# Kernel tuning notes

Hardware: AMD Instinct MI355X
Metric: run time of the kernel (lower is better)

The kernel has to match this reference:

```python
import jax, jax.numpy as jnp
import numpy as np

N_NODES = 50000
D_FEAT = 128
N_EDGES = 600000
HIDDEN = 256


def setup_inputs() -> dict:
    key = jax.random.key(0)
    k1, k2, k3, k4 = jax.random.split(key, 4)
    nodes = jax.random.normal(k1, (N_NODES, D_FEAT), dtype=jnp.float32)
    senders = jax.random.randint(k2, (N_EDGES,), 0, N_NODES, dtype=jnp.int32)
    receivers = jax.random.randint(k3, (N_EDGES,), 0, N_NODES, dtype=jnp.int32)
    # Dense(hidden): input dim = 2*D_FEAT (concat of aggregated + self features)
    W = jax.random.normal(k4, (2 * D_FEAT, HIDDEN), dtype=jnp.float32) / np.sqrt(2 * D_FEAT)
    b = jnp.zeros((HIDDEN,), dtype=jnp.float32)
    return {"nodes": nodes, "senders": senders, "receivers": receivers, "W": W, "b": b}


def reference(nodes, senders, receivers, W, b):
    n = nodes.shape[0]
    # segment_mean: gather sender features, scatter-sum onto receivers, divide by counts
    gathered = nodes[senders]                                    # [E, D]
    sums = jax.ops.segment_sum(gathered, receivers, num_segments=n)  # [N, D]
    counts = jax.ops.segment_sum(
        jnp.ones((senders.shape[0],), dtype=nodes.dtype), receivers, num_segments=n
    )                                                            # [N]
    h_e = sums / jnp.maximum(counts, 1.0)[:, None]               # mean (0 for empty segments)
    h = jnp.concatenate([h_e, nodes], axis=-1)                   # [N, 2D]
    out = jax.nn.relu(h @ W + b)                                 # [N, HIDDEN]
    return out
```

## Files before the change

### kernel.cpp

```cpp
#include <hip/hip_runtime.h>
#include <hip/hip_bf16.h>

#define N_NODES 50000
#define D_FEAT  128
#define N_EDGES 600000
#define HIDDEN  256
#define K_DIM   256

#define BUCKET   64
#define M_TILE   32
#define NTILES   1563
#define H_STRIDE 264

typedef __attribute__((ext_vector_type(8))) short bf16x8;
typedef __attribute__((ext_vector_type(4))) float f32x4;

__device__ __forceinline__ unsigned short f32_to_bf16(float f) {
    unsigned int u = __float_as_uint(f);
    unsigned int r = (u + 0x7fffu + ((u >> 16) & 1u)) >> 16;
    return (unsigned short)r;
}
__device__ __forceinline__ unsigned int pack_bf16x2(float lo, float hi) {
    return (unsigned int)f32_to_bf16(lo) | ((unsigned int)f32_to_bf16(hi) << 16);
}

__global__ __launch_bounds__(256) void build_and_repack(
    const int* __restrict__ senders,
    const int* __restrict__ receivers,
    const float* __restrict__ W,
    unsigned int* __restrict__ cnt,
    unsigned short* __restrict__ edges16,
    unsigned short* __restrict__ Wp) {
    const int gid = blockIdx.x * 256 + threadIdx.x;
    const int gsz = gridDim.x * 256;
    for (int e = gid; e < N_EDGES; e += gsz) {
        int r = receivers[e];
        unsigned int slot = atomicAdd(&cnt[r], 1u);
        if (slot < (unsigned int)BUCKET)
            edges16[(size_t)r * BUCKET + slot] = (unsigned short)senders[e];
    }
    for (int t = gid; t < 65536; t += gsz) {
        int kt = t >> 13;
        int n  = (t >> 5) & 255;
        int q  = (t >> 3) & 3;
        int j  = t & 7;
        int k  = kt * 32 + q * 8 + j;
        Wp[t] = f32_to_bf16(W[k * 256 + n]);
    }
}

__global__ __launch_bounds__(256) void gather_mean_gemm(
    const float* __restrict__ nodes,
    const unsigned int* __restrict__ cnt,
    const unsigned short* __restrict__ edges16,
    const unsigned short* __restrict__ Wp,
    const float* __restrict__ bias,
    float* __restrict__ out) {
    __shared__ __align__(16) unsigned int h32[M_TILE * (H_STRIDE / 2)];

    const int m0   = blockIdx.x * M_TILE;
    const int tid  = threadIdx.x;
    const int wave = tid >> 6;
    const int lane = tid & 63;

    for (int i = 0; i < 8; i++) {
        int row = wave * 8 + i;
        int m   = m0 + row;
        float s0 = 0.f, s1 = 0.f, p0 = 0.f, p1 = 0.f;
        float q0 = 0.f, q1 = 0.f, r0 = 0.f, r1 = 0.f;
        float self0 = 0.f, self1 = 0.f;
        unsigned int ec = 0;
        if (m < N_NODES) {
            unsigned int c = cnt[m];
            ec = c < (unsigned int)BUCKET ? c : (unsigned int)BUCKET;
            const unsigned int* ep =
                (const unsigned int*)(edges16 + (size_t)m * BUCKET);
            unsigned int np = ec >> 1;
            unsigned int pj = 0;
            for (; pj + 4 <= np; pj += 4) {
                unsigned int w0 = ep[pj + 0], w1 = ep[pj + 1];
                unsigned int w2 = ep[pj + 2], w3 = ep[pj + 3];
                const float2 va = *(const float2*)(nodes + (size_t)(w0 & 0xffffu) * D_FEAT + lane * 2);
                const float2 vb = *(const float2*)(nodes + (size_t)(w0 >> 16)     * D_FEAT + lane * 2);
                const float2 vc = *(const float2*)(nodes + (size_t)(w1 & 0xffffu) * D_FEAT + lane * 2);
                const float2 vd = *(const float2*)(nodes + (size_t)(w1 >> 16)     * D_FEAT + lane * 2);
                const float2 ve = *(const float2*)(nodes + (size_t)(w2 & 0xffffu) * D_FEAT + lane * 2);
                const float2 vf = *(const float2*)(nodes + (size_t)(w2 >> 16)     * D_FEAT + lane * 2);
                const float2 vg = *(const float2*)(nodes + (size_t)(w3 & 0xffffu) * D_FEAT + lane * 2);
                const float2 vh = *(const float2*)(nodes + (size_t)(w3 >> 16)     * D_FEAT + lane * 2);
                s0 += va.x; s1 += va.y;  p0 += vb.x; p1 += vb.y;
                q0 += vc.x; q1 += vc.y;  r0 += vd.x; r1 += vd.y;
                s0 += ve.x; s1 += ve.y;  p0 += vf.x; p1 += vf.y;
                q0 += vg.x; q1 += vg.y;  r0 += vh.x; r1 += vh.y;
            }
            for (; pj < np; pj++) {
                unsigned int w0 = ep[pj];
                const float2 va = *(const float2*)(nodes + (size_t)(w0 & 0xffffu) * D_FEAT + lane * 2);
                const float2 vb = *(const float2*)(nodes + (size_t)(w0 >> 16)     * D_FEAT + lane * 2);
                s0 += va.x; s1 += va.y;  p0 += vb.x; p1 += vb.y;
            }
            if (ec & 1u) {
                unsigned int sid = edges16[(size_t)m * BUCKET + (ec - 1)];
                const float2 va = *(const float2*)(nodes + (size_t)sid * D_FEAT + lane * 2);
                s0 += va.x; s1 += va.y;
            }
            const float2 sv = *(const float2*)(nodes + (size_t)m * D_FEAT + lane * 2);
            self0 = sv.x; self1 = sv.y;
        }
        float inv = 1.0f / fmaxf((float)ec, 1.0f);
        float a0 = (s0 + p0 + q0 + r0) * inv;
        float a1 = (s1 + p1 + q1 + r1) * inv;
        h32[row * (H_STRIDE / 2) + lane]      = pack_bf16x2(a0, a1);
        h32[row * (H_STRIDE / 2) + 64 + lane] = pack_bf16x2(self0, self1);
    }
    __syncthreads();

    const unsigned short* h = (const unsigned short*)h32;
    const int nbase = wave * 64;
    const int rsel  = lane & 15;
    const int quad  = lane >> 4;

    f32x4 acc[2][4] = {};

    for (int kk = 0; kk < K_DIM; kk += 32) {
        bf16x8 a[2], bw[4];
        #pragma unroll
        for (int mt = 0; mt < 2; mt++) {
            const unsigned short* pa =
                &h[(mt * 16 + rsel) * H_STRIDE + kk + quad * 8];
            a[mt] = *(const bf16x8*)pa;
        }
        int kt = kk >> 5;
        #pragma unroll
        for (int nt = 0; nt < 4; nt++) {
            int n = nbase + nt * 16 + rsel;
            bw[nt] = *(const bf16x8*)&Wp[kt * 8192 + n * 32 + quad * 8];
        }
        #pragma unroll
        for (int mt = 0; mt < 2; mt++)
            #pragma unroll
            for (int nt = 0; nt < 4; nt++)
                acc[mt][nt] = __builtin_amdgcn_mfma_f32_16x16x32_bf16(
                    a[mt], bw[nt], acc[mt][nt], 0, 0, 0);
    }

    #pragma unroll
    for (int nt = 0; nt < 4; nt++) {
        int n = nbase + nt * 16 + rsel;
        float bn = bias[n];
        #pragma unroll
        for (int mt = 0; mt < 2; mt++) {
            #pragma unroll
            for (int r = 0; r < 4; r++) {
                int m = m0 + mt * 16 + quad * 4 + r;
                if (m < N_NODES) {
                    float v = acc[mt][nt][r] + bn;
                    out[(size_t)m * HIDDEN + n] = fmaxf(v, 0.0f);
                }
            }
        }
    }
}

extern "C" void kernel_launch(void* const* d_in, const int* in_sizes, int n_in,
                              void* d_out, int out_size, void* d_ws, size_t ws_size,
                              hipStream_t stream) {
    const float* nodes     = (const float*)d_in[0];
    const int*   senders   = (const int*)d_in[1];
    const int*   receivers = (const int*)d_in[2];
    const float* W         = (const float*)d_in[3];
    const float* bias      = (const float*)d_in[4];
    float*       out       = (float*)d_out;

    unsigned int*   cnt     = (unsigned int*)d_ws;
    unsigned short* edges16 = (unsigned short*)(cnt + N_NODES);
    unsigned short* Wp      = edges16 + (size_t)N_NODES * BUCKET;

    hipMemsetAsync(cnt, 0, (size_t)N_NODES * sizeof(unsigned int), stream);

    build_and_repack<<<dim3((N_EDGES + 255) / 256), dim3(256), 0, stream>>>(
        senders, receivers, W, cnt, edges16, Wp);

    gather_mean_gemm<<<dim3(NTILES), dim3(256), 0, stream>>>(
        nodes, cnt, edges16, Wp, bias, out);
}
```

Before: 199.6 us.

## Gather from bf16 node copy with tile-flattened edge list and LDS atomics

```diff
diff --git a/kernel.cpp b/kernel.cpp
--- a/kernel.cpp
+++ b/kernel.cpp
@@ -10,7 +10,6 @@
 #define BUCKET   64
 #define M_TILE   32
 #define NTILES   1563
-#define H_STRIDE 264
 
 typedef __attribute__((ext_vector_type(8))) short bf16x8;
 typedef __attribute__((ext_vector_type(4))) float f32x4;
@@ -20,16 +19,21 @@
     unsigned int r = (u + 0x7fffu + ((u >> 16) & 1u)) >> 16;
     return (unsigned short)r;
 }
+__device__ __forceinline__ float bf16_to_f32(unsigned short u) {
+    return __uint_as_float(((unsigned int)u) << 16);
+}
 __device__ __forceinline__ unsigned int pack_bf16x2(float lo, float hi) {
     return (unsigned int)f32_to_bf16(lo) | ((unsigned int)f32_to_bf16(hi) << 16);
 }
 
-__global__ __launch_bounds__(256) void build_and_repack(
+__global__ __launch_bounds__(256) void build_conv_repack(
     const int* __restrict__ senders,
     const int* __restrict__ receivers,
+    const float* __restrict__ nodes,
     const float* __restrict__ W,
     unsigned int* __restrict__ cnt,
     unsigned short* __restrict__ edges16,
+    unsigned int* __restrict__ nb,
     unsigned short* __restrict__ Wp) {
     const int gid = blockIdx.x * 256 + threadIdx.x;
     const int gsz = gridDim.x * 256;
@@ -39,6 +43,10 @@
         if (slot < (unsigned int)BUCKET)
             edges16[(size_t)r * BUCKET + slot] = (unsigned short)senders[e];
     }
+    for (int p = gid; p < N_NODES * 64; p += gsz) {
+        const float2 v = *(const float2*)(nodes + (size_t)p * 2);
+        nb[p] = pack_bf16x2(v.x, v.y);
+    }
     for (int t = gid; t < 65536; t += gsz) {
         int kt = t >> 13;
         int n  = (t >> 5) & 255;
@@ -49,88 +57,119 @@
     }
 }
 
-__global__ __launch_bounds__(256) void gather_mean_gemm(
-    const float* __restrict__ nodes,
+__global__ __launch_bounds__(256, 4) void gather_mean_gemm(
+    const unsigned int* __restrict__ nb,
     const unsigned int* __restrict__ cnt,
     const unsigned short* __restrict__ edges16,
     const unsigned short* __restrict__ Wp,
     const float* __restrict__ bias,
     float* __restrict__ out) {
-    __shared__ __align__(16) unsigned int h32[M_TILE * (H_STRIDE / 2)];
+    __shared__ __align__(16) float hacc[M_TILE * 132];
+    __shared__ __align__(16) unsigned int shared2[M_TILE * 68];
+    __shared__ unsigned int cn[M_TILE];
+    __shared__ unsigned int pref[M_TILE + 1];
+    __shared__ float invdeg[M_TILE];
 
     const int m0   = blockIdx.x * M_TILE;
     const int tid  = threadIdx.x;
     const int wave = tid >> 6;
     const int lane = tid & 63;
 
-    for (int i = 0; i < 8; i++) {
-        int row = wave * 8 + i;
-        int m   = m0 + row;
-        float s0 = 0.f, s1 = 0.f, p0 = 0.f, p1 = 0.f;
-        float q0 = 0.f, q1 = 0.f, r0 = 0.f, r1 = 0.f;
-        float self0 = 0.f, self1 = 0.f;
-        unsigned int ec = 0;
+    for (int i = tid; i < M_TILE * 132; i += 256) hacc[i] = 0.f;
+    if (tid < M_TILE) {
+        int m = m0 + tid;
+        unsigned int c = 0;
         if (m < N_NODES) {
-            unsigned int c = cnt[m];
-            ec = c < (unsigned int)BUCKET ? c : (unsigned int)BUCKET;
-            const unsigned int* ep =
-                (const unsigned int*)(edges16 + (size_t)m * BUCKET);
-            unsigned int np = ec >> 1;
-            unsigned int pj = 0;
-            for (; pj + 4 <= np; pj += 4) {
-                unsigned int w0 = ep[pj + 0], w1 = ep[pj + 1];
-                unsigned int w2 = ep[pj + 2], w3 = ep[pj + 3];
-                const float2 va = *(const float2*)(nodes + (size_t)(w0 & 0xffffu) * D_FEAT + lane * 2);
-                const float2 vb = *(const float2*)(nodes + (size_t)(w0 >> 16)     * D_FEAT + lane * 2);
-                const float2 vc = *(const float2*)(nodes + (size_t)(w1 & 0xffffu) * D_FEAT + lane * 2);
-                const float2 vd = *(const float2*)(nodes + (size_t)(w1 >> 16)     * D_FEAT + lane * 2);
-                const float2 ve = *(const float2*)(nodes + (size_t)(w2 & 0xffffu) * D_FEAT + lane * 2);
-                const float2 vf = *(const float2*)(nodes + (size_t)(w2 >> 16)     * D_FEAT + lane * 2);
-                const float2 vg = *(const float2*)(nodes + (size_t)(w3 & 0xffffu) * D_FEAT + lane * 2);
-                const float2 vh = *(const float2*)(nodes + (size_t)(w3 >> 16)     * D_FEAT + lane * 2);
-                s0 += va.x; s1 += va.y;  p0 += vb.x; p1 += vb.y;
-                q0 += vc.x; q1 += vc.y;  r0 += vd.x; r1 += vd.y;
-                s0 += ve.x; s1 += ve.y;  p0 += vf.x; p1 += vf.y;
-                q0 += vg.x; q1 += vg.y;  r0 += vh.x; r1 += vh.y;
-            }
-            for (; pj < np; pj++) {
-                unsigned int w0 = ep[pj];
-                const float2 va = *(const float2*)(nodes + (size_t)(w0 & 0xffffu) * D_FEAT + lane * 2);
-                const float2 vb = *(const float2*)(nodes + (size_t)(w0 >> 16)     * D_FEAT + lane * 2);
-                s0 += va.x; s1 += va.y;  p0 += vb.x; p1 += vb.y;
-            }
-            if (ec & 1u) {
-                unsigned int sid = edges16[(size_t)m * BUCKET + (ec - 1)];
-                const float2 va = *(const float2*)(nodes + (size_t)sid * D_FEAT + lane * 2);
-                s0 += va.x; s1 += va.y;
-            }
-            const float2 sv = *(const float2*)(nodes + (size_t)m * D_FEAT + lane * 2);
-            self0 = sv.x; self1 = sv.y;
-        }
-        float inv = 1.0f / fmaxf((float)ec, 1.0f);
-        float a0 = (s0 + p0 + q0 + r0) * inv;
-        float a1 = (s1 + p1 + q1 + r1) * inv;
-        h32[row * (H_STRIDE / 2) + lane]      = pack_bf16x2(a0, a1);
-        h32[row * (H_STRIDE / 2) + 64 + lane] = pack_bf16x2(self0, self1);
-    }
-    __syncthreads();
-
-    const unsigned short* h = (const unsigned short*)h32;
+            c = cnt[m];
+            if (c > (unsigned int)BUCKET) c = (unsigned int)BUCKET;
+        }
+        cn[tid] = c;
+        invdeg[tid] = 1.0f / fmaxf((float)c, 1.0f);
+    }
+    __syncthreads();
+    if (tid == 0) {
+        unsigned int run = 0;
+        for (int r = 0; r < M_TILE; r++) { pref[r] = run; run += cn[r]; }
+        pref[M_TILE] = run;
+    }
+    __syncthreads();
+
+    unsigned int* eflat = shared2;
+    {
+        int r  = tid >> 3, st = tid & 7;
+        unsigned int c = cn[r], base = pref[r];
+        size_t eb = (size_t)(m0 + r) * BUCKET;
+        for (unsigned int s = st; s < c; s += 8)
+            eflat[base + s] = ((unsigned int)r << 16) | edges16[eb + s];
+    }
+    __syncthreads();
+
+    const unsigned short* nb16 = (const unsigned short*)nb;
+    const int total = pref[M_TILE];
+    for (int base = wave * 16; base < total; base += 64) {
+        int nEdge = total - base; if (nEdge > 16) nEdge = 16;
+        unsigned int desc[16];
+        unsigned short flo[16], fhi[16];
+        #pragma unroll
+        for (int j = 0; j < 16; j++) {
+            if (j < nEdge) {
+                desc[j] = eflat[base + j];
+                size_t sa = (size_t)(desc[j] & 0xffffu) * 128;
+                flo[j] = nb16[sa + lane];
+                fhi[j] = nb16[sa + 64 + lane];
+            }
+        }
+        #pragma unroll
+        for (int j = 0; j < 16; j++) {
+            if (j < nEdge) {
+                int r = (int)(desc[j] >> 16);
+                atomicAdd(&hacc[r * 132 + lane],      bf16_to_f32(flo[j]));
+                atomicAdd(&hacc[r * 132 + 64 + lane], bf16_to_f32(fhi[j]));
+            }
+        }
+    }
+    __syncthreads();
+
+    for (int i = tid; i < M_TILE * 128; i += 256) {
+        int r = i >> 7, c = i & 127;
+        hacc[r * 132 + c] *= invdeg[r];
+    }
+    for (int i = tid; i < M_TILE * 64; i += 256) {
+        int r = i >> 6, c = i & 63;
+        int m = m0 + r;
+        shared2[r * 68 + c] = (m < N_NODES) ? nb[(size_t)m * 64 + c] : 0u;
+    }
+    __syncthreads();
+
+    const unsigned short* hs16 = (const unsigned short*)shared2;
     const int nbase = wave * 64;
     const int rsel  = lane & 15;
     const int quad  = lane >> 4;
 
     f32x4 acc[2][4] = {};
 
-    for (int kk = 0; kk < K_DIM; kk += 32) {
+    #pragma unroll
+    for (int kt = 0; kt < 8; kt++) {
         bf16x8 a[2], bw[4];
         #pragma unroll
         for (int mt = 0; mt < 2; mt++) {
-            const unsigned short* pa =
-                &h[(mt * 16 + rsel) * H_STRIDE + kk + quad * 8];
-            a[mt] = *(const bf16x8*)pa;
-        }
-        int kt = kk >> 5;
+            int row = mt * 16 + rsel;
+            if (kt < 4) {
+                const float* pa = &hacc[row * 132 + kt * 32 + quad * 8];
+                f32x4 vlo = *(const f32x4*)pa;
+                f32x4 vhi = *(const f32x4*)(pa + 4);
+                union { bf16x8 v; unsigned short u[8]; } tmp;
+                #pragma unroll
+                for (int j = 0; j < 4; j++) {
+                    tmp.u[j]     = f32_to_bf16(vlo[j]);
+                    tmp.u[4 + j] = f32_to_bf16(vhi[j]);
+                }
+                a[mt] = tmp.v;
+            } else {
+                a[mt] = *(const bf16x8*)
+                    &hs16[row * 136 + (kt - 4) * 32 + quad * 8];
+            }
+        }
         #pragma unroll
         for (int nt = 0; nt < 4; nt++) {
             int n = nbase + nt * 16 + rsel;
@@ -174,13 +213,14 @@
 
     unsigned int*   cnt     = (unsigned int*)d_ws;
     unsigned short* edges16 = (unsigned short*)(cnt + N_NODES);
-    unsigned short* Wp      = edges16 + (size_t)N_NODES * BUCKET;
+    unsigned int*   nb      = (unsigned int*)(edges16 + (size_t)N_NODES * BUCKET);
+    unsigned short* Wp      = (unsigned short*)(nb + (size_t)N_NODES * 64);
 
     hipMemsetAsync(cnt, 0, (size_t)N_NODES * sizeof(unsigned int), stream);
 
-    build_and_repack<<<dim3((N_EDGES + 255) / 256), dim3(256), 0, stream>>>(
-        senders, receivers, W, cnt, edges16, Wp);
+    build_conv_repack<<<dim3(4096), dim3(256), 0, stream>>>(
+        senders, receivers, nodes, W, cnt, edges16, nb, Wp);
 
     gather_mean_gemm<<<dim3(NTILES), dim3(256), 0, stream>>>(
-        nodes, cnt, edges16, Wp, bias, out);
-}
+        nb, cnt, edges16, Wp, bias, out);
+}
```

Result: slower. 592.5 us (+196.8%).

## Convert node features to bf16 once and gather in padded 16-wide batches

Applied to the files above, without the earlier changes.

```diff
diff --git a/kernel.cpp b/kernel.cpp
--- a/kernel.cpp
+++ b/kernel.cpp
@@ -8,6 +8,7 @@
 #define K_DIM   256
 
 #define BUCKET   64
+#define ZERO_ROW 50000
 #define M_TILE   32
 #define NTILES   1563
 #define H_STRIDE 264
@@ -23,13 +24,21 @@
 __device__ __forceinline__ unsigned int pack_bf16x2(float lo, float hi) {
     return (unsigned int)f32_to_bf16(lo) | ((unsigned int)f32_to_bf16(hi) << 16);
 }
-
-__global__ __launch_bounds__(256) void build_and_repack(
+__device__ __forceinline__ float bf_lo(unsigned int v) {
+    return __uint_as_float(v << 16);
+}
+__device__ __forceinline__ float bf_hi(unsigned int v) {
+    return __uint_as_float(v & 0xffff0000u);
+}
+
+__global__ __launch_bounds__(256) void build_conv_repack(
     const int* __restrict__ senders,
     const int* __restrict__ receivers,
+    const float* __restrict__ nodes,
     const float* __restrict__ W,
+    unsigned short* __restrict__ edges16,
     unsigned int* __restrict__ cnt,
-    unsigned short* __restrict__ edges16,
+    unsigned int* __restrict__ nb,
     unsigned short* __restrict__ Wp) {
     const int gid = blockIdx.x * 256 + threadIdx.x;
     const int gsz = gridDim.x * 256;
@@ -39,6 +48,11 @@
         if (slot < (unsigned int)BUCKET)
             edges16[(size_t)r * BUCKET + slot] = (unsigned short)senders[e];
     }
+    for (int p = gid; p < N_NODES * 64; p += gsz) {
+        const float2 v = *(const float2*)(nodes + (size_t)p * 2);
+        nb[p] = pack_bf16x2(v.x, v.y);
+    }
+    if (gid < 64) nb[(size_t)ZERO_ROW * 64 + gid] = 0u;
     for (int t = gid; t < 65536; t += gsz) {
         int kt = t >> 13;
         int n  = (t >> 5) & 255;
@@ -50,7 +64,7 @@
 }
 
 __global__ __launch_bounds__(256) void gather_mean_gemm(
-    const float* __restrict__ nodes,
+    const unsigned int* __restrict__ nb,
     const unsigned int* __restrict__ cnt,
     const unsigned short* __restrict__ edges16,
     const unsigned short* __restrict__ Wp,
@@ -68,50 +82,67 @@
         int m   = m0 + row;
         float s0 = 0.f, s1 = 0.f, p0 = 0.f, p1 = 0.f;
         float q0 = 0.f, q1 = 0.f, r0 = 0.f, r1 = 0.f;
-        float self0 = 0.f, self1 = 0.f;
-        unsigned int ec = 0;
+        unsigned int selfp = 0u;
+        unsigned int c = 0;
         if (m < N_NODES) {
-            unsigned int c = cnt[m];
-            ec = c < (unsigned int)BUCKET ? c : (unsigned int)BUCKET;
+            c = cnt[m];
+            if (c > (unsigned int)BUCKET) c = (unsigned int)BUCKET;
             const unsigned int* ep =
                 (const unsigned int*)(edges16 + (size_t)m * BUCKET);
-            unsigned int np = ec >> 1;
-            unsigned int pj = 0;
-            for (; pj + 4 <= np; pj += 4) {
-                unsigned int w0 = ep[pj + 0], w1 = ep[pj + 1];
-                unsigned int w2 = ep[pj + 2], w3 = ep[pj + 3];
-                const float2 va = *(const float2*)(nodes + (size_t)(w0 & 0xffffu) * D_FEAT + lane * 2);
-                const float2 vb = *(const float2*)(nodes + (size_t)(w0 >> 16)     * D_FEAT + lane * 2);
-                const float2 vc = *(const float2*)(nodes + (size_t)(w1 & 0xffffu) * D_FEAT + lane * 2);
-                const float2 vd = *(const float2*)(nodes + (size_t)(w1 >> 16)     * D_FEAT + lane * 2);
-                const float2 ve = *(const float2*)(nodes + (size_t)(w2 & 0xffffu) * D_FEAT + lane * 2);
-                const float2 vf = *(const float2*)(nodes + (size_t)(w2 >> 16)     * D_FEAT + lane * 2);
-                const float2 vg = *(const float2*)(nodes + (size_t)(w3 & 0xffffu) * D_FEAT + lane * 2);
-                const float2 vh = *(const float2*)(nodes + (size_t)(w3 >> 16)     * D_FEAT + lane * 2);
-                s0 += va.x; s1 += va.y;  p0 += vb.x; p1 += vb.y;
-                q0 += vc.x; q1 += vc.y;  r0 += vd.x; r1 += vd.y;
-                s0 += ve.x; s1 += ve.y;  p0 += vf.x; p1 += vf.y;
-                q0 += vg.x; q1 += vg.y;  r0 += vh.x; r1 += vh.y;
+            unsigned int cp = (c + 15u) & ~15u;
+            for (unsigned int s = 0; s < cp; s += 16) {
+                unsigned int w0 = ep[(s >> 1) + 0], w1 = ep[(s >> 1) + 1];
+                unsigned int w2 = ep[(s >> 1) + 2], w3 = ep[(s >> 1) + 3];
+                unsigned int w4 = ep[(s >> 1) + 4], w5 = ep[(s >> 1) + 5];
+                unsigned int w6 = ep[(s >> 1) + 6], w7 = ep[(s >> 1) + 7];
+                unsigned int id0  = (s + 0  < c) ? (w0 & 0xffffu) : ZERO_ROW;
+                unsigned int id1  = (s + 1  < c) ? (w0 >> 16)     : ZERO_ROW;
+                unsigned int id2  = (s + 2  < c) ? (w1 & 0xffffu) : ZERO_ROW;
+                unsigned int id3  = (s + 3  < c) ? (w1 >> 16)     : ZERO_ROW;
+                unsigned int id4  = (s + 4  < c) ? (w2 & 0xffffu) : ZERO_ROW;
+                unsigned int id5  = (s + 5  < c) ? (w2 >> 16)     : ZERO_ROW;
+                unsigned int id6  = (s + 6  < c) ? (w3 & 0xffffu) : ZERO_ROW;
+                unsigned int id7  = (s + 7  < c) ? (w3 >> 16)     : ZERO_ROW;
+                unsigned int id8  = (s + 8  < c) ? (w4 & 0xffffu) : ZERO_ROW;
+                unsigned int id9  = (s + 9  < c) ? (w4 >> 16)     : ZERO_ROW;
+                unsigned int id10 = (s + 10 < c) ? (w5 & 0xffffu) : ZERO_ROW;
+                unsigned int id11 = (s + 11 < c) ? (w5 >> 16)     : ZERO_ROW;
+                unsigned int id12 = (s + 12 < c) ? (w6 & 0xffffu) : ZERO_ROW;
+                unsigned int id13 = (s + 13 < c) ? (w6 >> 16)     : ZERO_ROW;
+                unsigned int id14 = (s + 14 < c) ? (w7 & 0xffffu) : ZERO_ROW;
+                unsigned int id15 = (s + 15 < c) ? (w7 >> 16)     : ZERO_ROW;
+                unsigned int v0  = nb[(size_t)id0  * 64 + lane];
+                unsigned int v1  = nb[(size_t)id1  * 64 + lane];
+                unsigned int v2  = nb[(size_t)id2  * 64 + lane];
+                unsigned int v3  = nb[(size_t)id3  * 64 + lane];
+                unsigned int v4  = nb[(size_t)id4  * 64 + lane];
+                unsigned int v5  = nb[(size_t)id5  * 64 + lane];
+                unsigned int v6  = nb[(size_t)id6  * 64 + lane];
+                unsigned int v7  = nb[(size_t)id7  * 64 + lane];
+                unsigned int v8  = nb[(size_t)id8  * 64 + lane];
+                unsigned int v9  = nb[(size_t)id9  * 64 + lane];
+                unsigned int v10 = nb[(size_t)id10 * 64 + lane];
+                unsigned int v11 = nb[(size_t)id11 * 64 + lane];
+                unsigned int v12 = nb[(size_t)id12 * 64 + lane];
+                unsigned int v13 = nb[(size_t)id13 * 64 + lane];
+                unsigned int v14 = nb[(size_t)id14 * 64 + lane];
+                unsigned int v15 = nb[(size_t)id15 * 64 + lane];
+                s0 += bf_lo(v0);  s1 += bf_hi(v0);  p0 += bf_lo(v1);  p1 += bf_hi(v1);
+                q0 += bf_lo(v2);  q1 += bf_hi(v2);  r0 += bf_lo(v3);  r1 += bf_hi(v3);
+                s0 += bf_lo(v4);  s1 += bf_hi(v4);  p0 += bf_lo(v5);  p1 += bf_hi(v5);
+                q0 += bf_lo(v6);  q1 += bf_hi(v6);  r0 += bf_lo(v7);  r1 += bf_hi(v7);
+                s0 += bf_lo(v8);  s1 += bf_hi(v8);  p0 += bf_lo(v9);  p1 += bf_hi(v9);
+                q0 += bf_lo(v10); q1 += bf_hi(v10); r0 += bf_lo(v11); r1 += bf_hi(v11);
+                s0 += bf_lo(v12); s1 += bf_hi(v12); p0 += bf_lo(v13); p1 += bf_hi(v13);
+                q0 += bf_lo(v14); q1 += bf_hi(v14); r0 += bf_lo(v15); r1 += bf_hi(v15);
             }
-            for (; pj < np; pj++) {
-                unsigned int w0 = ep[pj];
-                const float2 va = *(const float2*)(nodes + (size_t)(w0 & 0xffffu) * D_FEAT + lane * 2);
-                const float2 vb = *(const float2*)(nodes + (size_t)(w0 >> 16)     * D_FEAT + lane * 2);
-                s0 += va.x; s1 += va.y;  p0 += vb.x; p1 += vb.y;
-            }
-            if (ec & 1u) {
-                unsigned int sid = edges16[(size_t)m * BUCKET + (ec - 1)];
-                const float2 va = *(const float2*)(nodes + (size_t)sid * D_FEAT + lane * 2);
-                s0 += va.x; s1 += va.y;
-            }
-            const float2 sv = *(const float2*)(nodes + (size_t)m * D_FEAT + lane * 2);
-            self0 = sv.x; self1 = sv.y;
-        }
-        float inv = 1.0f / fmaxf((float)ec, 1.0f);
+            selfp = nb[(size_t)m * 64 + lane];
+        }
+        float inv = 1.0f / fmaxf((float)c, 1.0f);
         float a0 = (s0 + p0 + q0 + r0) * inv;
         float a1 = (s1 + p1 + q1 + r1) * inv;
         h32[row * (H_STRIDE / 2) + lane]      = pack_bf16x2(a0, a1);
-        h32[row * (H_STRIDE / 2) + 64 + lane] = pack_bf16x2(self0, self1);
+        h32[row * (H_STRIDE / 2) + 64 + lane] = selfp;
     }
     __syncthreads();
 
@@ -172,15 +203,16 @@
     const float* bias      = (const float*)d_in[4];
     float*       out       = (float*)d_out;
 
-    unsigned int*   cnt     = (unsigned int*)d_ws;
-    unsigned short* edges16 = (unsigned short*)(cnt + N_NODES);
-    unsigned short* Wp      = edges16 + (size_t)N_NODES * BUCKET;
+    unsigned short* edges16 = (unsigned short*)d_ws;
+    unsigned int*   cnt     = (unsigned int*)(edges16 + (size_t)N_NODES * BUCKET);
+    unsigned int*   nb      = cnt + N_NODES;
+    unsigned short* Wp      = (unsigned short*)(nb + (size_t)(N_NODES + 1) * 64);
 
     hipMemsetAsync(cnt, 0, (size_t)N_NODES * sizeof(unsigned int), stream);
 
-    build_and_repack<<<dim3((N_EDGES + 255) / 256), dim3(256), 0, stream>>>(
-        senders, receivers, W, cnt, edges16, Wp);
+    build_conv_repack<<<dim3(1024), dim3(256), 0, stream>>>(
+        senders, receivers, nodes, W, edges16, cnt, nb, Wp);
 
     gather_mean_gemm<<<dim3(NTILES), dim3(256), 0, stream>>>(
-        nodes, cnt, edges16, Wp, bias, out);
-}
+        nb, cnt, edges16, Wp, bias, out);
+}
```

New measurement: 182.1 us. 8.8% less time.
